# Optimization experiments

Hardware: AMD Instinct MI355X
Metric: run time of the kernel (lower is better)

The kernel has to match this reference:

```python
import jax, jax.numpy as jnp
import numpy as np

HEADS, DIM_HEAD = 4, 32
EAF_LAMBDA, EAF_ZMAX = 1.0, 4.0
MIN_SIGMA, MAX_SIGMA = 1.0, 8.0

def _gen_grid(h, w):
    xs = np.linspace(0.0, 1.0, w, dtype=np.float32)
    ys = np.linspace(0.0, 1.0, h, dtype=np.float32)
    gy, gx = np.meshgrid(ys, xs, indexing='ij')
    return np.stack([gx, gy, np.ones_like(gx)], 0)  # [3,h,w]

def setup_inputs():
    key = jax.random.key(0)
    ks = jax.random.split(key, 12)
    B, N, C, D = 4, 6, 128, 128
    Hb, Wb, fh, fw = 25, 25, 24, 48
    inner = HEADS * DIM_HEAD
    # BEV ego-plane grid (same math as BEVEmbedding with bev 200x200, 100m, 3 decoder blocks)
    g = _gen_grid(Hb, Wb)
    g[0] *= 200.0
    g[1] *= 200.0
    V = np.array([[0., -2., 100.], [-2., 0., 100.], [0., 0., 1.]], dtype=np.float32)
    bev_grid = (np.linalg.inv(V) @ g.reshape(3, -1)).reshape(3, Hb, Wb)
    # image plane pixel grid (buffer), scaled to 480x224 image
    ip = _gen_grid(fh, fw)[None]
    ip[:, 0] *= 480.0
    ip[:, 1] *= 224.0
    # cam->world extrinsics: 6 surround cameras on a ring
    E_inv = np.zeros((B, N, 4, 4), dtype=np.float32)
    for n in range(N):
        yaw = 2.0 * np.pi * n / N
        c, s = np.cos(yaw), np.sin(yaw)
        E_inv[:, n, :3, :3] = np.array([[c, -s, 0.], [s, c, 0.], [0., 0., 1.]], dtype=np.float32)
        E_inv[:, n, :3, 3] = np.array([2. * c, 2. * s, 1.6], dtype=np.float32)
        E_inv[:, n, 3, 3] = 1.0
    Kmat = np.array([[260., 0., 240.], [0., 260., 112.], [0., 0., 1.]], dtype=np.float32)
    I_inv = np.broadcast_to(np.linalg.inv(Kmat), (B, N, 3, 3)).astype(np.float32).copy()
    w = lambda k, shape: 0.02 * jax.random.normal(k, shape, dtype=jnp.float32)
    return dict(
        x=jax.random.normal(ks[0], (B, D, Hb, Wb), dtype=jnp.float32),
        feature=jax.random.normal(ks[1], (B, N, C, fh, fw), dtype=jnp.float32),
        I_inv=jnp.asarray(I_inv), E_inv=jnp.asarray(E_inv),
        bev_grid=jnp.asarray(bev_grid), image_plane=jnp.asarray(ip),
        bn_v_g=jnp.ones(C), bn_v_b=jnp.zeros(C), bn_v_m=jnp.zeros(C), bn_v_var=jnp.ones(C),
        conv_v_w=w(ks[2], (D, C)),
        bn_k_g=jnp.ones(C), bn_k_b=jnp.zeros(C), bn_k_m=jnp.zeros(C), bn_k_var=jnp.ones(C),
        conv_k_w=w(ks[3], (D, C)),
        ln_q_g=jnp.ones(D), ln_q_b=jnp.zeros(D),
        ln_k_g=jnp.ones(D), ln_k_b=jnp.zeros(D),
        ln_v_g=jnp.ones(D), ln_v_b=jnp.zeros(D),
        Wq=w(ks[4], (inner, D)), bq=jnp.zeros(inner),
        Wk=w(ks[5], (inner, D)), bk=jnp.zeros(inner),
        Wv=w(ks[6], (inner, D)), bv=jnp.zeros(inner),
        Wo=w(ks[7], (D, inner)), bo=jnp.zeros(D),
        ln_pre_g=jnp.ones(D), ln_pre_b=jnp.zeros(D),
        W1=w(ks[8], (2 * D, D)), b1=jnp.zeros(2 * D),
        W2=w(ks[9], (D, 2 * D)), b2=jnp.zeros(D),
        ln_post_g=jnp.ones(D), ln_post_b=jnp.zeros(D),
    )

def _ln(x, g, b):
    m = x.mean(-1, keepdims=True)
    v = ((x - m) ** 2).mean(-1, keepdims=True)
    return (x - m) * jax.lax.rsqrt(v + 1e-5) * g + b

def _bn_relu_conv(f, g, b, mu, var, Wc):
    # inference BatchNorm2d -> ReLU -> 1x1 Conv (no bias)
    f = (f - mu[None, :, None, None]) * (jax.lax.rsqrt(var + 1e-5) * g)[None, :, None, None] + b[None, :, None, None]
    f = jax.nn.relu(f)
    return jnp.einsum('bchw,dc->bdhw', f, Wc)

def reference(x, feature, I_inv, E_inv, bev_grid, image_plane,
              bn_v_g, bn_v_b, bn_v_m, bn_v_var, conv_v_w,
              bn_k_g, bn_k_b, bn_k_m, bn_k_var, conv_k_w,
              ln_q_g, ln_q_b, ln_k_g, ln_k_b, ln_v_g, ln_v_b,
              Wq, bq, Wk, bk, Wv, bv, Wo, bo,
              ln_pre_g, ln_pre_b, W1, b1, W2, b2, ln_post_g, ln_post_b):
    B, N, C, fh, fw = feature.shape
    _, D, Hb, Wb = x.shape
    Q = Hb * Wb
    Kp = fh * fw
    feat = feature.reshape(B * N, C, fh, fw)
    val = _bn_relu_conv(feat, bn_v_g, bn_v_b, bn_v_m, bn_v_var, conv_v_w)
    keyf = _bn_relu_conv(feat, bn_k_g, bn_k_b, bn_k_m, bn_k_var, conv_k_w)
    v = val.reshape(B, N, D, fh, fw)
    k = keyf.reshape(B, N, D, fh, fw)
    # ---- EAF weights ----
    xy = bev_grid[:2].reshape(2, Q).T                      # [Q,2]
    ones = jnp.ones((Q, 1), dtype=bev_grid.dtype)
    P0 = jnp.concatenate([xy, 0.0 * ones, ones], -1)       # [Q,4] z=0
    P1 = jnp.concatenate([xy, EAF_ZMAX * ones, ones], -1)  # [Q,4] z=zmax
    E = jnp.linalg.inv(E_inv)                              # world->cam
    P0c = jnp.einsum('bnij,qj->bnqi', E, P0)
    P1c = jnp.einsum('bnij,qj->bnqi', E, P1)
    Icam = jnp.linalg.inv(I_inv)
    p0 = jnp.einsum('bnij,bnqj->bnqi', Icam, P0c[..., :3])
    p1 = jnp.einsum('bnij,bnqj->bnqi', Icam, P1c[..., :3])
    p0 = p0 / (p0[..., 2:3] + 1e-8)
    p1 = p1 / (p1[..., 2:3] + 1e-8)
    l = jnp.cross(p0, p1)                                  # epipolar line [B,N,Q,3]
    denom = jnp.maximum(jnp.sqrt(l[..., 0] ** 2 + l[..., 1] ** 2), 1e-8)
    l_hat = l / denom[..., None]
    x_img = image_plane[0].reshape(3, Kp).T                # [K,3]
    d = jnp.abs(jnp.einsum('bnqj,kj->bnqk', l_hat, x_img))
    # adaptive lambda_{q,i}
    cam_xy = E_inv[..., :2, 3]                             # [B,N,2]
    vec = xy[None, None] - cam_xy[:, :, None]              # [B,N,Q,2]
    dist = jnp.linalg.norm(vec, axis=-1) + 1e-6
    dist_max = dist.max(axis=(1, 2), keepdims=True) + 1e-6
    dist_norm = jnp.clip(dist / dist_max, 0.0, 1.0)
    sigma = MAX_SIGMA - dist_norm * (MAX_SIGMA - MIN_SIGMA)
    lambda_qi = 1.0 / (sigma + 1e-6)
    scale_w = (EAF_LAMBDA * lambda_qi) ** 2                # [B,N,Q]
    Wmask = jnp.exp(-scale_w[..., None] * d ** 2)          # [B,N,Q,K]
    W_logits = Wmask.transpose(0, 2, 1, 3).reshape(B, Q, N * Kp)
    # ---- cross attention (EAF weight multiplied into logits pre-softmax) ----
    qt = x.reshape(B, D, Q).transpose(0, 2, 1)             # [B,Q,D]
    kt = k.transpose(0, 1, 3, 4, 2).reshape(B, N * Kp, D)
    vt = v.transpose(0, 1, 3, 4, 2).reshape(B, N * Kp, D)
    qp = _ln(qt, ln_q_g, ln_q_b) @ Wq.T + bq
    kp = _ln(kt, ln_k_g, ln_k_b) @ Wk.T + bk
    vp = _ln(vt, ln_v_g, ln_v_b) @ Wv.T + bv
    qh = qp.reshape(B, Q, HEADS, DIM_HEAD).transpose(0, 2, 1, 3)
    kh = kp.reshape(B, N * Kp, HEADS, DIM_HEAD).transpose(0, 2, 1, 3)
    vh = vp.reshape(B, N * Kp, HEADS, DIM_HEAD).transpose(0, 2, 1, 3)
    logits = jnp.einsum('bhqd,bhkd->bhqk', qh, kh) * (DIM_HEAD ** -0.5)
    logits = logits * W_logits[:, None]                    # broadcast over heads
    attn = jax.nn.softmax(logits, axis=-1)
    out = jnp.einsum('bhqk,bhkd->bhqd', attn, vh)
    out = out.transpose(0, 2, 1, 3).reshape(B, Q, HEADS * DIM_HEAD)
    out = out @ Wo.T + bo                                  # [B,Q,D]
    z = out + qt                                           # skip = x
    z = _ln(z, ln_pre_g, ln_pre_b)
    z = z + (jax.nn.gelu(z @ W1.T + b1, approximate=False) @ W2.T + b2)
    z = _ln(z, ln_post_g, ln_post_b)
    return z.transpose(0, 2, 1).reshape(B, D, Hb, Wb)
```

## Files before the change

kernel.cpp:

```cpp
#include <hip/hip_runtime.h>
#include <hip/hip_bf16.h>

typedef unsigned short u16;
typedef __attribute__((ext_vector_type(8))) short short8v;
typedef __attribute__((ext_vector_type(4))) float f32x4;
typedef __attribute__((ext_vector_type(2))) __fp16 fp16x2;

#define B_   4
#define N_   6
#define Q_   625
#define QPAD 640
#define KP_  1152
#define NK_  6912
#define NKB  216
#define NSPLIT 12
#define KSEG (NK_/NSPLIT)
#define FHW  1152
#define LOG2E 1.4426950408889634f
#define LOG2_LOG2E 0.5287663729448977f

__device__ __forceinline__ float bfu(unsigned int u16v){ return __uint_as_float(u16v << 16); }
__device__ __forceinline__ unsigned int f2bfu(float f){
  unsigned int u = __float_as_uint(f);
  return (u + 0x7fffu + ((u>>16)&1u)) >> 16;
// ... 110 lines not shown
    for (int j=0;j<4;++j) a[i][4+j] = (i==j)?1.f:0.f;
  }
  #pragma unroll
  for (int col=0;col<4;++col){
    float inv = 1.f/a[col][col];
    #pragma unroll
    for (int j=0;j<8;++j) a[col][j]*=inv;
    #pragma unroll
    for (int rr=0;rr<4;++rr) if (rr!=col){
      float f=a[rr][col];
      #pragma unroll
      for (int j=0;j<8;++j) a[rr][j] -= f*a[col][j];
    }
  }
  float E[3][4];
  #pragma unroll
  for (int i=0;i<3;++i)
    #pragma unroll
    for (int j=0;j<4;++j) E[i][j]=a[i][4+j];

  float m9[9];
  #pragma unroll
  for (int i=0;i<9;++i) m9[i] = Iinv[(b*N_+n)*9 + i];
  float c00 =  m9[4]*m9[8]-m9[5]*m9[7];
  float c01 = -(m9[3]*m9[8]-m9[5]*m9[6]);
  float c02 =  m9[3]*m9[7]-m9[4]*m9[6];
  float id = 1.f/(m9[0]*c00 + m9[1]*c01 + m9[2]*c02);
  float Ic[3][3];
  Ic[0][0]=c00*id; Ic[0][1]=-(m9[1]*m9[8]-m9[2]*m9[7])*id; Ic[0][2]=(m9[1]*m9[5]-m9[2]*m9[4])*id;
  Ic[1][0]=c01*id; Ic[1][1]= (m9[0]*m9[8]-m9[2]*m9[6])*id; Ic[1][2]=-(m9[0]*m9[5]-m9[2]*m9[3])*id;
  Ic[2][0]=c02*id; Ic[2][1]=-(m9[0]*m9[7]-m9[1]*m9[6])*id; Ic[2][2]=(m9[0]*m9[4]-m9[1]*m9[3])*id;

  float x = bev[q], y = bev[Q_+q];
  float P0c[3], P1c[3];
  #pragma unroll
  for (int i=0;i<3;++i){
    P0c[i] = E[i][0]*x + E[i][1]*y + E[i][3];
    P1c[i] = E[i][0]*x + E[i][1]*y + E[i][2]*4.0f + E[i][3];
  }
  float p0[3], p1[3];
  #pragma unroll
  for (int i=0;i<3;++i){
    p0[i] = Ic[i][0]*P0c[0] + Ic[i][1]*P0c[1] + Ic[i][2]*P0c[2];
    p1[i] = Ic[i][0]*P1c[0] + Ic[i][1]*P1c[1] + Ic[i][2]*P1c[2];
  }
  float z0 = p0[2]+1e-8f, z1 = p1[2]+1e-8f;
  #pragma unroll
  for (int i=0;i<3;++i){ p0[i]/=z0; p1[i]/=z1; }
  float l0 = p0[1]*p1[2]-p0[2]*p1[1];
  float l1 = p0[2]*p1[0]-p0[0]*p1[2];
  float l2 = p0[0]*p1[1]-p0[1]*p1[0];
  float den = fmaxf(sqrtf(l0*l0+l1*l1), 1e-8f);
  float cx = Einv[(b*N_+n)*16+3], cy = Einv[(b*N_+n)*16+7];
  float dx = x-cx, dy = y-cy;
  float dist = sqrtf(dx*dx+dy*dy) + 1e-6f;
  float dn = fminf(fmaxf(dist/dmax[b], 0.f), 1.f);
  float sigma = 8.0f - dn*7.0f;
  float lam = 1.f/(sigma+1e-6f);
  float* g = geom + (size_t)idx*4;
  g[0]=l0/den; g[1]=l1/den; g[2]=l2/den;
  g[3]=-(lam*lam)*LOG2E;
}

__global__ __launch_bounds__(256) void k_kvproj(
  const void* __restrict__ feat, const unsigned* __restrict__ magic,
  const float* __restrict__ csK, const float* __restrict__ cbK,
  const float* __restrict__ csV, const float* __restrict__ cbV,
  const u16* __restrict__ convKbf, const u16* __restrict__ convVbf,
  const u16* __restrict__ WkBf, const u16* __restrict__ WvBf,
  const float* __restrict__ lkg, const float* __restrict__ lkb,
  const float* __restrict__ lvg, const float* __restrict__ lvb,
  const float* __restrict__ bk_, const float* __restrict__ bv_,
  u16* __restrict__ kp, u16* __restrict__ vpB)
{
  __shared__ __align__(16) unsigned char lds_tile[16384];
  __shared__ float2 redLN[4][64];
  uint4* lds16 = reinterpret_cast<uint4*>(lds_tile);

  const int tid = threadIdx.x;
  const int w = tid >> 6, l = tid & 63;
  const int lr = l & 15, lg4 = l >> 4;
  const int ptile = blockIdx.x;
  const int bn = blockIdx.y, b = bn/6, n = bn - b*6;
  const int half = blockIdx.z;
  const bool isbf = (*magic == 0x3F803F80u);

  const float* cs   = half ? csV : csK;
  const float* cbv_ = half ? cbV : cbK;
  const u16* convB  = half ? convVbf : convKbf;
  const u16* WB     = half ? WvBf : WkBf;
  const float* lng  = half ? lvg : lkg;
  const float* lnb  = half ? lvb : lkb;
  const float* bias = half ? bv_ : bk_;

  const size_t fbase = (size_t)bn*128*FHW + ptile*64 + l;
  const int psw = l & 7;
  #pragma unroll
  for (int pass=0; pass<4; ++pass){
    int c0 = pass*32 + w*8;
    unsigned int u[4];
    #pragma unroll
    for (int i2=0;i2<4;++i2){
      int ca = c0 + i2*2, cb2 = ca+1;
      float fa = ldfeat(feat, fbase + (size_t)ca*FHW, isbf);
      float fb = ldfeat(feat, fbase + (size_t)cb2*FHW, isbf);
      float aa = fmaxf(fa*cs[ca]+cbv_[ca], 0.f);
      float ab = fmaxf(fb*cs[cb2]+cbv_[cb2], 0.f);
      u[i2] = f2bfu(aa) | (f2bfu(ab)<<16);
    }
    int c8 = c0 >> 3;
    lds16[l*16 + (c8 ^ psw)] = make_uint4(u[0],u[1],u[2],u[3]);
  }
  __syncthreads();

  f32x4 acc[2][4];
  #pragma unroll
  for (int i=0;i<2;++i)
    #pragma unroll
    for (int j=0;j<4;++j) acc[i][j] = (f32x4){0.f,0.f,0.f,0.f};

  #pragma unroll
  for (int ks2=0; ks2<4; ++ks2){
    short8v af[2];
    #pragma unroll
    for (int ib=0; ib<2; ++ib)
      af[ib] = *reinterpret_cast<const short8v*>(convB + ((w*32 + ib*16 + lr)<<7) + (ks2<<5) + (lg4<<3));
    #pragma unroll
    for (int pb2=0; pb2<4; ++pb2){
      int p = pb2*16 + lr;
      U4S8 bu; bu.u = lds16[p*16 + ((ks2*4 + lg4) ^ (p&7))];
      acc[0][pb2] = __builtin_amdgcn_mfma_f32_16x16x32_bf16(af[0], bu.s, acc[0][pb2], 0,0,0);
      acc[1][pb2] = __builtin_amdgcn_mfma_f32_16x16x32_bf16(af[1], bu.s, acc[1][pb2], 0,0,0);
    }
  }

  float s1v[4], s2v[4];
  #pragma unroll
  for (int pb2=0;pb2<4;++pb2){
    float s=0.f, s2=0.f;
    #pragma unroll
    for (int ib=0;ib<2;++ib)
      #pragma unroll
      for (int r=0;r<4;++r){ float v = acc[ib][pb2][r]; s+=v; s2+=v*v; }
    s += __shfl_xor(s,16);  s += __shfl_xor(s,32);
    s2 += __shfl_xor(s2,16); s2 += __shfl_xor(s2,32);
    s1v[pb2]=s; s2v[pb2]=s2;
  }
  if (l < 16){
    #pragma unroll
    for (int pb2=0;pb2<4;++pb2) redLN[w][pb2*16+l] = make_float2(s1v[pb2], s2v[pb2]);
  }
  __syncthreads();

  float mean[4], rstd[4];
  #pragma unroll
  for (int pb2=0;pb2<4;++pb2){
    int p = pb2*16 + lr;
    float2 t0 = redLN[0][p], t1 = redLN[1][p], t2 = redLN[2][p], t3 = redLN[3][p];
    float S = t0.x+t1.x+t2.x+t3.x, S2 = t0.y+t1.y+t2.y+t3.y;
    float mm = S*(1.f/128.f);
    float var = fmaxf(S2*(1.f/128.f) - mm*mm, 0.f);
    mean[pb2] = mm; rstd[pb2] = rsqrtf(var + 1e-5f);
  }
  float4 g4[2], b4[2];
  #pragma unroll
  for (int ib=0;ib<2;++ib){
    g4[ib] = *reinterpret_cast<const float4*>(lng + w*32 + ib*16 + lg4*4);
    b4[ib] = *reinterpret_cast<const float4*>(lnb + w*32 + ib*16 + lg4*4);
  }
  #pragma unroll
  for (int ib=0;ib<2;++ib){
    const float* gg = &g4[ib].x; const float* bb2 = &b4[ib].x;
    int d0 = w*32 + ib*16 + lg4*4;
    int d8 = d0 >> 3, doff = (d0 & 7) * 2;
    #pragma unroll
    for (int pb2=0;pb2<4;++pb2){
      int p = pb2*16 + lr;
      float z0 = (acc[ib][pb2][0]-mean[pb2])*rstd[pb2]*gg[0]+bb2[0];
      float z1 = (acc[ib][pb2][1]-mean[pb2])*rstd[pb2]*gg[1]+bb2[1];
      float z2 = (acc[ib][pb2][2]-mean[pb2])*rstd[pb2]*gg[2]+bb2[2];
      float z3 = (acc[ib][pb2][3]-mean[pb2])*rstd[pb2]*gg[3]+bb2[3];
      unsigned int u0 = f2bfu(z0) | (f2bfu(z1)<<16);
      unsigned int u1 = f2bfu(z2) | (f2bfu(z3)<<16);
      *reinterpret_cast<uint2*>(lds_tile + p*256 + ((d8 ^ (p&7))<<4) + doff) = make_uint2(u0,u1);
    }
  }
  __syncthreads();

  f32x4 acc2[2][4];
  #pragma unroll
  for (int i=0;i<2;++i)
    #pragma unroll
    for (int j=0;j<4;++j) acc2[i][j] = (f32x4){0.f,0.f,0.f,0.f};

  #pragma unroll
  for (int ks2=0; ks2<4; ++ks2){
    short8v af[2];
    #pragma unroll
    for (int ib=0; ib<2; ++ib)
      af[ib] = *reinterpret_cast<const short8v*>(WB + ((w*32 + ib*16 + lr)<<7) + (ks2<<5) + (lg4<<3));
    #pragma unroll
    for (int pb2=0; pb2<4; ++pb2){
      int p = pb2*16 + lr;
      U4S8 bu; bu.u = lds16[p*16 + ((ks2*4 + lg4) ^ (p&7))];
      acc2[0][pb2] = __builtin_amdgcn_mfma_f32_16x16x32_bf16(af[0], bu.s, acc2[0][pb2], 0,0,0);
      acc2[1][pb2] = __builtin_amdgcn_mfma_f32_16x16x32_bf16(af[1], bu.s, acc2[1][pb2], 0,0,0);
    }
  }
  float4 bias4[2];
  #pragma unroll
  for (int ib=0;ib<2;++ib)
    bias4[ib] = *reinterpret_cast<const float4*>(bias + w*32 + ib*16 + lg4*4);

  __syncthreads();

  if (half == 0){
    #pragma unroll
    for (int ib=0;ib<2;++ib){
      const float* bb2 = &bias4[ib].x;
      int i0 = w*32 + ib*16 + lg4*4;
      int i8 = i0 >> 3, ioff = (i0 & 7) * 2;
      #pragma unroll
      for (int pb2=0;pb2<4;++pb2){
        int p = pb2*16 + lr;
        unsigned int u0 = f2bfu(acc2[ib][pb2][0]+bb2[0]) | (f2bfu(acc2[ib][pb2][1]+bb2[1])<<16);
        unsigned int u1 = f2bfu(acc2[ib][pb2][2]+bb2[2]) | (f2bfu(acc2[ib][pb2][3]+bb2[3])<<16);
        *reinterpret_cast<uint2*>(lds_tile + p*256 + ((i8 ^ (p&7))<<4) + ioff) = make_uint2(u0,u1);
      }
    }
    __syncthreads();
    size_t krow0 = (size_t)b*NK_ + n*KP_ + ptile*64;
    #pragma unroll
    for (int kk=0;kk<4;++kk){
      int idx = kk*256 + tid;
      int p = idx >> 4, j = idx & 15;
      uint4 vv = lds16[p*16 + (j ^ (p&7))];
      *reinterpret_cast<uint4*>(kp + (krow0 + p)*128 + j*8) = vv;
    }
  } else {
    u16* lds2 = reinterpret_cast<u16*>(lds_tile);
    #pragma unroll
    for (int ib=0;ib<2;++ib){
      const float* bb2 = &bias4[ib].x;
      int i0 = w*32 + ib*16 + lg4*4;
      #pragma unroll
      for (int pb2=0;pb2<4;++pb2){
        int p = pb2*16 + lr;
        int pc = ((p&12)<<1) | (p&3) | ((p&16)>>2) | (p&32);
        #pragma unroll
        for (int r=0;r<4;++r)
          lds2[(i0+r)*64 + pc] = (u16)f2bfu(acc2[ib][pb2][r]+bb2[r]);
      }
    }
    __syncthreads();
    int kb0 = b*NKB + n*(KP_/32) + ptile*2;
    #pragma unroll
    for (int kk=0;kk<4;++kk){
      int idx = kk*256 + tid;
      int p2 = idx >> 9, d = (idx>>2)&127, ch = idx&3;
      uint4 vv = lds16[d*8 + p2*4 + ch];
      *reinterpret_cast<uint4*>(vpB + ((size_t)(kb0+p2)*128 + d)*32 + ch*8) = vv;
    }
  }
}

__global__ __launch_bounds__(256) void k_qprojM(
  const float* __restrict__ x, const float* __restrict__ lg, const float* __restrict__ lb,
  const u16* __restrict__ WqBf, const float* __restrict__ bq_, u16* __restrict__ qp)
{
  const float SCL = 0.17677669529663687f;
  __shared__ __align__(16) unsigned char lds_tile[16384];
  __shared__ float redS[4][64], redS2[4][64];
  uint4* lds16 = reinterpret_cast<uint4*>(lds_tile);

  const int tid = threadIdx.x;
  const int w = tid >> 6, l = tid & 63;
  const int lr = l & 15, lg4 = l >> 4;
  const int q0 = blockIdx.x * 64;
  const int b  = blockIdx.y;

  int qg = q0 + l; if (qg > Q_-1) qg = Q_-1;
  float xv[32];
  float s = 0.f, s2 = 0.f;
  #pragma unroll
  for (int i=0;i<32;++i){
    float v = x[(size_t)(b*128 + w*32 + i)*Q_ + qg];
    xv[i] = v; s += v; s2 += v*v;
  }
  redS[w][l] = s; redS2[w][l] = s2;
  __syncthreads();
  float S  = redS[0][l]+redS[1][l]+redS[2][l]+redS[3][l];
  float S2 = redS2[0][l]+redS2[1][l]+redS2[2][l]+redS2[3][l];
  float mm = S*(1.f/128.f);
  float rs = rsqrtf(fmaxf(S2*(1.f/128.f)-mm*mm, 0.f) + 1e-5f);
  #pragma unroll
  for (int j=0;j<4;++j){
    unsigned u[4];
    #pragma unroll
    for (int c2=0;c2<4;++c2){
      int i = j*8 + c2*2;
      int d = w*32 + i;
      float z0 = (xv[i]  -mm)*rs*lg[d]   + lb[d];
      float z1 = (xv[i+1]-mm)*rs*lg[d+1] + lb[d+1];
      u[c2] = f2bfu(z0) | (f2bfu(z1)<<16);
    }
    int d8 = w*4 + j;
    lds16[l*16 + (d8 ^ (l&7))] = make_uint4(u[0],u[1],u[2],u[3]);
  }
  __syncthreads();

  f32x4 acc2[2][4];
  #pragma unroll
  for (int i=0;i<2;++i)
    #pragma unroll
    for (int j=0;j<4;++j) acc2[i][j] = (f32x4){0.f,0.f,0.f,0.f};

  #pragma unroll
  for (int ks2=0; ks2<4; ++ks2){
    short8v af[2];
    #pragma unroll
    for (int ib=0; ib<2; ++ib)
      af[ib] = *reinterpret_cast<const short8v*>(WqBf + ((w*32 + ib*16 + lr)<<7) + (ks2<<5) + (lg4<<3));
    #pragma unroll
    for (int pb2=0; pb2<4; ++pb2){
      int p = pb2*16 + lr;
      U4S8 bu; bu.u = lds16[p*16 + ((ks2*4 + lg4) ^ (p&7))];
      acc2[0][pb2] = __builtin_amdgcn_mfma_f32_16x16x32_bf16(af[0], bu.s, acc2[0][pb2], 0,0,0);
      acc2[1][pb2] = __builtin_amdgcn_mfma_f32_16x16x32_bf16(af[1], bu.s, acc2[1][pb2], 0,0,0);
    }
  }
  float4 bias4[2];
  #pragma unroll
  for (int ib=0;ib<2;++ib)
    bias4[ib] = *reinterpret_cast<const float4*>(bq_ + w*32 + ib*16 + lg4*4);

  __syncthreads();
  #pragma unroll
  for (int ib=0;ib<2;++ib){
    const float* bb2 = &bias4[ib].x;
    int i0 = w*32 + ib*16 + lg4*4;
    int i8 = i0 >> 3, ioff = (i0 & 7) * 2;
    #pragma unroll
    for (int pb2=0;pb2<4;++pb2){
      int p = pb2*16 + lr;
      unsigned int u0 = f2bfu((acc2[ib][pb2][0]+bb2[0])*SCL) | (f2bfu((acc2[ib][pb2][1]+bb2[1])*SCL)<<16);
      unsigned int u1 = f2bfu((acc2[ib][pb2][2]+bb2[2])*SCL) | (f2bfu((acc2[ib][pb2][3]+bb2[3])*SCL)<<16);
      *reinterpret_cast<uint2*>(lds_tile + p*256 + ((i8 ^ (p&7))<<4) + ioff) = make_uint2(u0,u1);
    }
  }
  __syncthreads();
  #pragma unroll
  for (int kk=0;kk<4;++kk){
    int idx = kk*256 + tid;
    int p = idx >> 4, j = idx & 15;
    uint4 vv = lds16[p*16 + (j ^ (p&7))];
    *reinterpret_cast<uint4*>(qp + (size_t)(b*QPAD + q0 + p)*128 + j*8) = vv;
  }
}

__global__ __launch_bounds__(256) void k_attn(
    const u16* __restrict__ qp, const u16* __restrict__ kp, const u16* __restrict__ vpB,
    const float* __restrict__ geom, const float* __restrict__ ip,
    float* __restrict__ part)
{
  __shared__ uint4 ldsK[2][512];
  __shared__ uint4 ldsV[2][512];
  __shared__ u16  ldsW[2][32*36];

  const int tid = threadIdx.x;
  const int h = tid >> 6;
  const int lane = tid & 63;
  const int lq = lane & 15;
  const int g  = lane >> 4;
  const int bid = blockIdx.x;
  const int b = bid / (20*NSPLIT);
  const int r = bid - b*(20*NSPLIT);
  const int qt = r / NSPLIT;
  const int ks = r - qt*NSPLIT;
  const int q0 = qt*32;
  const int qa = q0 + lq;
  const int qb = q0 + 16 + lq;

  short8v bq0 = *reinterpret_cast<const short8v*>(qp + ((size_t)(b*QPAD + qa))*128 + h*32 + g*8);
  short8v bq1 = *reinterpret_cast<const short8v*>(qp + ((size_t)(b*QPAD + qb))*128 + h*32 + g*8);

  f32x4 o00={0,0,0,0}, o01={0,0,0,0}, o10={0,0,0,0}, o11={0,0,0,0};
  f32x4 zero4 = {0.f,0.f,0.f,0.f};
  float psum0 = 0.f, psum1 = 0.f;

  const int kbeg = ks*KSEG, kend = kbeg + KSEG;
  const int n0 = kbeg / KP_;
  const int pb0 = kbeg - n0*KP_;

  const int wq = tid >> 3, wc = tid & 7;
  int qwg = q0 + wq; if (qwg > Q_-1) qwg = Q_-1;
  const float* gw_ = geom + ((size_t)((b*N_+n0)*Q_ + qwg))*4;
  const float wl0 = gw_[0], wl1 = gw_[1], wl2 = gw_[2], wgw = gw_[3];

  const int c2 = tid*2;
  const int kr0 = c2 >> 4, kch = c2 & 15;
  const int vd0 = c2 >> 2, vch = c2 & 3;
  const int vsw = (vd0 >> 1) & 3;
  auto STAGE = [&](int buf, int k0){
    const uint4* gk = reinterpret_cast<const uint4*>(kp + (size_t)(b*NK_ + k0)*128);
    uint4 k0v = gk[c2], k1v = gk[c2+1];
    ldsK[buf][kr0*16 + (kch     ^ (kr0&7))] = k0v;
    ldsK[buf][kr0*16 + ((kch+1) ^ (kr0&7))] = k1v;
    const uint4* gv = reinterpret_cast<const uint4*>(vpB + ((size_t)(b*NKB + (k0>>5))*128)*32);
    uint4 v0v = gv[c2], v1v = gv[c2+1];
    ldsV[buf][vd0*4 + (vch     ^ vsw)] = v0v;
    ldsV[buf][vd0*4 + ((vch+1) ^ vsw)] = v1v;
  };
  auto WSTAGE = [&](int buf, int k0){
    int key = pb0 + (k0 - kbeg) + wc*4;
    float4 xx = *reinterpret_cast<const float4*>(ip + key);
    float4 yy = *reinterpret_cast<const float4*>(ip + KP_ + key);
    const float* xp = &xx.x; const float* yp = &yy.x;
    float wv[4];
    #pragma unroll
    for (int i=0;i<4;++i){
      float dln = fmaf(wl0, xp[i], fmaf(wl1, yp[i], wl2));
      wv[i] = exp2a(fmaf(wgw, dln*dln, LOG2_LOG2E));
    }
    uint2 pk;
    pk.x = cvtpk_f16(wv[0], wv[1]);
    pk.y = cvtpk_f16(wv[2], wv[3]);
    *reinterpret_cast<uint2*>(&ldsW[buf][wq*36 + wc*4]) = pk;
  };

  STAGE(0, kbeg);
  WSTAGE(0, kbeg);

  int cur = 0;
  const int kchunk = h*4 + g;
  const int dd = h*32 + lq;
  const int vswr = (dd >> 1) & 3;
  for (int k0 = kbeg; k0 < kend; k0 += 32){
    __syncthreads();
    bool more = (k0 + 32) < kend;
    if (more){ STAGE(cur^1, k0+32); WSTAGE(cur^1, k0+32); }

    uint2 wA0 = *reinterpret_cast<const uint2*>(&ldsW[cur][lq*36 + g*4]);
    uint2 wA1 = *reinterpret_cast<const uint2*>(&ldsW[cur][lq*36 + 16 + g*4]);
    uint2 wB0 = *reinterpret_cast<const uint2*>(&ldsW[cur][(16+lq)*36 + g*4]);
    uint2 wB1 = *reinterpret_cast<const uint2*>(&ldsW[cur][(16+lq)*36 + 16 + g*4]);
    float w00[4], w01[4], w10[4], w11[4];
    {
      H2U t0,t1,t2,t3,t4,t5,t6,t7;
      t0.u=wA0.x; t1.u=wA0.y; t2.u=wA1.x; t3.u=wA1.y;
      t4.u=wB0.x; t5.u=wB0.y; t6.u=wB1.x; t7.u=wB1.y;
      w00[0]=(float)t0.h[0]; w00[1]=(float)t0.h[1]; w00[2]=(float)t1.h[0]; w00[3]=(float)t1.h[1];
      w01[0]=(float)t2.h[0]; w01[1]=(float)t2.h[1]; w01[2]=(float)t3.h[0]; w01[3]=(float)t3.h[1];
      w10[0]=(float)t4.h[0]; w10[1]=(float)t4.h[1]; w10[2]=(float)t5.h[0]; w10[3]=(float)t5.h[1];
      w11[0]=(float)t6.h[0]; w11[1]=(float)t6.h[1]; w11[2]=(float)t7.h[0]; w11[3]=(float)t7.h[1];
    }

    __builtin_amdgcn_s_setprio(1);
    U4S8 a0, a1;
    a0.u = ldsK[cur][lq*16      + (kchunk ^ (lq&7))];
    a1.u = ldsK[cur][(16+lq)*16 + (kchunk ^ (lq&7))];
    f32x4 s00 = __builtin_amdgcn_mfma_f32_16x16x32_bf16(a0.s, bq0, zero4, 0,0,0);
    f32x4 s01 = __builtin_amdgcn_mfma_f32_16x16x32_bf16(a1.s, bq0, zero4, 0,0,0);
    f32x4 s10 = __builtin_amdgcn_mfma_f32_16x16x32_bf16(a0.s, bq1, zero4, 0,0,0);
    f32x4 s11 = __builtin_amdgcn_mfma_f32_16x16x32_bf16(a1.s, bq1, zero4, 0,0,0);

    float p00[4], p01[4], p10[4], p11[4];
    #pragma unroll
    for (int r2=0;r2<4;++r2){
      p00[r2] = exp2a(fmaf(s00[r2], w00[r2], -8.f));
      p01[r2] = exp2a(fmaf(s01[r2], w01[r2], -8.f));
      psum0 += p00[r2] + p01[r2];
      p10[r2] = exp2a(fmaf(s10[r2], w10[r2], -8.f));
      p11[r2] = exp2a(fmaf(s11[r2], w11[r2], -8.f));
      psum1 += p10[r2] + p11[r2];
    }
    union { short8v s; unsigned int u[4]; } bp0, bp1;
    bp0.u[0] = cvtpk_bf16(p00[0], p00[1]);
    bp0.u[1] = cvtpk_bf16(p00[2], p00[3]);
    bp0.u[2] = cvtpk_bf16(p01[0], p01[1]);
    bp0.u[3] = cvtpk_bf16(p01[2], p01[3]);
    bp1.u[0] = cvtpk_bf16(p10[0], p10[1]);
    bp1.u[1] = cvtpk_bf16(p10[2], p10[3]);
    bp1.u[2] = cvtpk_bf16(p11[0], p11[1]);
    bp1.u[3] = cvtpk_bf16(p11[2], p11[3]);

    U4S8 v0, v1;
    v0.u = ldsV[cur][dd*4      + (g ^ vswr)];
    v1.u = ldsV[cur][(dd+16)*4 + (g ^ vswr)];
    o00 = __builtin_amdgcn_mfma_f32_16x16x32_bf16(v0.s, bp0.s, o00, 0,0,0);
    o01 = __builtin_amdgcn_mfma_f32_16x16x32_bf16(v1.s, bp0.s, o01, 0,0,0);
    o10 = __builtin_amdgcn_mfma_f32_16x16x32_bf16(v0.s, bp1.s, o10, 0,0,0);
    o11 = __builtin_amdgcn_mfma_f32_16x16x32_bf16(v1.s, bp1.s, o11, 0,0,0);
    __builtin_amdgcn_s_setprio(0);

    cur ^= 1;
  }
  psum0 += __shfl_xor(psum0,16);
  psum0 += __shfl_xor(psum0,32);
  psum1 += __shfl_xor(psum1,16);
  psum1 += __shfl_xor(psum1,32);
  int slot0 = ((b*4 + h)*40 + qt*2    )*NSPLIT + ks;
  int slot1 = ((b*4 + h)*40 + qt*2 + 1)*NSPLIT + ks;
  float* pr0 = part + ((size_t)slot0*16 + lq)*34;
  float* pr1 = part + ((size_t)slot1*16 + lq)*34;
  #pragma unroll
  for (int r2=0;r2<4;++r2){
    pr0[g*4+r2] = o00[r2]; pr0[16+g*4+r2] = o01[r2];
    pr1[g*4+r2] = o10[r2]; pr1[16+g*4+r2] = o11[r2];
  }
  if (g==0){ pr0[33] = psum0; pr1[33] = psum1; }
}

__global__ __launch_bounds__(256) void k_epiM(
  const float* __restrict__ part, const float* __restrict__ x,
  const u16* __restrict__ WoBf, const float* __restrict__ bo_,
  const float* __restrict__ lpg, const float* __restrict__ lpb,
  const u16* __restrict__ W1Bf, const float* __restrict__ b1_,
  const u16* __restrict__ W2Bf, const float* __restrict__ b2_,
  const float* __restrict__ lsg, const float* __restrict__ lsb,
  void* __restrict__ out, const unsigned* __restrict__ magic)
{
  const float ISQ2 = 0.7071067811865476f;
  __shared__ __align__(16) unsigned char lds_tile[16384];
  __shared__ __align__(16) unsigned char lds_h1[32768];
  __shared__ float2 redLN[4][64];
  uint4* lds16 = reinterpret_cast<uint4*>(lds_tile);
  uint4* ldsH  = reinterpret_cast<uint4*>(lds_h1);

  const int tid = threadIdx.x;
  const int w = tid >> 6, l = tid & 63;
  const int lr = l & 15, lg4 = l >> 4;
  const int q0 = blockIdx.x * 64;
  const int b  = blockIdx.y;
  const bool isbf = (*magic == 0x3F803F80u);

  {
    int qg = q0 + l; if (qg > Q_-1) qg = Q_-1;
    int qt = qg >> 4, qq = qg & 15;
    const float* base = part + (size_t)(((b*4+w)*40+qt)*NSPLIT)*544 + qq*34;
    float den = 0.f;
    #pragma unroll
    for (int s=0;s<NSPLIT;++s) den += base[s*544 + 33];
    float rden = 1.f/den;
    float num[32];
    #pragma unroll
    for (int i=0;i<32;++i) num[i]=0.f;
    #pragma unroll
    for (int s=0;s<NSPLIT;++s){
      const float* bp = base + s*544;
      #pragma unroll
      for (int i=0;i<32;++i) num[i] += bp[i];
    }
    #pragma unroll
    for (int j=0;j<4;++j){
      unsigned u[4];
      #pragma unroll
      for (int c2=0;c2<4;++c2){
        int i = j*8 + c2*2;
        u[c2] = f2bfu(num[i]*rden) | (f2bfu(num[i+1]*rden)<<16);
      }
      int d8 = w*4 + j;
      lds16[l*16 + (d8 ^ (l&7))] = make_uint4(u[0],u[1],u[2],u[3]);
    }
  }
  __syncthreads();

  f32x4 acc[2][4];
  #pragma unroll
  for (int i=0;i<2;++i)
    #pragma unroll
    for (int j=0;j<4;++j) acc[i][j] = (f32x4){0.f,0.f,0.f,0.f};
  #pragma unroll
  for (int ks2=0; ks2<4; ++ks2){
    short8v af[2];
    #pragma unroll
    for (int ib=0; ib<2; ++ib)
      af[ib] = *reinterpret_cast<const short8v*>(WoBf + ((w*32 + ib*16 + lr)<<7) + (ks2<<5) + (lg4<<3));
// ... 202 lines not shown
  InPack P;
  int nseg = n_in < 38 ? n_in : 38;
  int c = 0;
  for (int i=0;i<nseg;++i){
    P.p[i] = d_in[i];
    P.off[i] = c;
    P.sz[i] = (i == 1) ? 0 : in_sizes[i];
    c += (P.sz[i] + 7) & ~7;
  }
  P.nseg = nseg;
  P.total = c;

  float* fw = (float*)d_ws;
  float* fin = fw;
  const float* fx    = fin + P.off[0];
  const float* fIinv = fin + P.off[2];
  const float* fEinv = fin + P.off[3];
  const float* fbev  = fin + P.off[4];
  const float* fip   = fin + P.off[5];
  const float* fbvg  = fin + P.off[6];
  const float* fbvb  = fin + P.off[7];
  const float* fbvm  = fin + P.off[8];
  const float* fbvv  = fin + P.off[9];
  const float* fcvw  = fin + P.off[10];
  const float* fbkg  = fin + P.off[11];
  const float* fbkb  = fin + P.off[12];
  const float* fbkm  = fin + P.off[13];
  const float* fbkv  = fin + P.off[14];
  const float* fckw  = fin + P.off[15];
  const float* flqg  = fin + P.off[16];
  const float* flqb  = fin + P.off[17];
  const float* flkg  = fin + P.off[18];
  const float* flkb  = fin + P.off[19];
  const float* flvg  = fin + P.off[20];
  const float* flvb  = fin + P.off[21];
  const float* fWq   = fin + P.off[22];
  const float* fbq   = fin + P.off[23];
  const float* fWk   = fin + P.off[24];
  const float* fbk   = fin + P.off[25];
  const float* fWv   = fin + P.off[26];
  const float* fbv   = fin + P.off[27];
  const float* fWo   = fin + P.off[28];
  const float* fbo   = fin + P.off[29];
  const float* flpg  = fin + P.off[30];
  const float* flpb  = fin + P.off[31];
  const float* fW1   = fin + P.off[32];
  const float* fb1   = fin + P.off[33];
  const float* fW2   = fin + P.off[34];
  const float* fb2   = fin + P.off[35];
  const float* flsg  = fin + P.off[36];
  const float* flsb  = fin + P.off[37];

  size_t off = (size_t)P.total;
  float* geomW = fin + off;  off += 60000;
  float* dmaxW = fin + off;  off += 8;
  float* csK = fin + off;    off += 128;
  float* cbK = fin + off;    off += 128;
  float* csV = fin + off;    off += 128;
  float* cbV = fin + off;    off += 128;
  float* part = fin + off;   off += (size_t)B_*4*40*NSPLIT*544;
  u16* bb = (u16*)(fin + off);
  u16* convKbf = bb;
  u16* convVbf = bb + 16384;
  u16* WkBf    = bb + 32768;
  u16* WvBf    = bb + 49152;
  u16* WqBf    = bb + 65536;
  u16* WoBf    = bb + 81920;
  u16* W1Bf    = bb + 98304;
  u16* W2Bf    = bb + 131072;
  u16* kp  = bb + 163840;
  u16* vpB = kp + (size_t)B_*NK_*128;
  u16* qp  = vpB + (size_t)B_*NK_*128;

  const unsigned* magic = (const unsigned*)d_in[6];
  const void* featRaw = d_in[1];

  k_ingest<<<(P.total+255)/256,256,0,stream>>>(P, fin, magic);
  k_prep<<<641,256,0,stream>>>(fckw,fcvw,fWk,fWv,fWq,fWo,fW1,fW2,
                               fbkg,fbkb,fbkm,fbkv, fbvg,fbvb,fbvm,fbvv,
                               convKbf,convVbf,WkBf,WvBf,WqBf,WoBf,W1Bf,W2Bf,
                               csK,cbK,csV,cbV);
  k_distmax<<<4,256,0,stream>>>(fbev, fEinv, dmaxW);
  k_geom<<<59,256,0,stream>>>(fEinv, fIinv, fbev, dmaxW, geomW);
  k_kvproj<<<dim3(18,24,2),256,0,stream>>>(featRaw, magic, csK,cbK,csV,cbV, convKbf,convVbf,
                                           WkBf,WvBf, flkg,flkb,flvg,flvb, fbk,fbv, kp, vpB);
  k_qprojM<<<dim3(10,B_),256,0,stream>>>(fx, flqg,flqb, WqBf, fbq, qp);
  k_attn<<<B_*20*NSPLIT,256,0,stream>>>(qp, kp, vpB, geomW, fip, part);
  k_epiM<<<dim3(10,B_),256,0,stream>>>(part, fx, WoBf,fbo, flpg,flpb, W1Bf,fb1, W2Bf,fb2,
                                       flsg,flsb, d_out, magic);
}
```

Measured before the change: 105.0 us.

## Merge K/V projection blocks to reuse feature loads; read V from global in attention

The K/V projection kernel now runs one block per tile that loops over both halves. It loads the 128-channel feature column into registers once instead of twice, which halves feature reads but halves the grid size and serialises the two projections. In the attention kernel, the LDS staging buffer for V is removed. Each lane now loads its V fragment directly from the pre-swizzled global layout, prefetched one iteration ahead in registers. This cuts LDS traffic and shared memory but leans on cache hits for V.

```diff
diff --git a/kernel.cpp b/kernel.cpp
--- a/kernel.cpp
+++ b/kernel.cpp
@@ -216,185 +216,194 @@
   const int lr = l & 15, lg4 = l >> 4;
   const int ptile = blockIdx.x;
   const int bn = blockIdx.y, b = bn/6, n = bn - b*6;
-  const int half = blockIdx.z;
   const bool isbf = (*magic == 0x3F803F80u);
 
-  const float* cs   = half ? csV : csK;
-  const float* cbv_ = half ? cbV : cbK;
-  const u16* convB  = half ? convVbf : convKbf;
-  const u16* WB     = half ? WvBf : WkBf;
-  const float* lng  = half ? lvg : lkg;
-  const float* lnb  = half ? lvb : lkb;
-  const float* bias = half ? bv_ : bk_;
-
   const size_t fbase = (size_t)bn*128*FHW + ptile*64 + l;
+  float fv[32];
+  #pragma unroll
+  for (int pass=0; pass<4; ++pass)
+    #pragma unroll
+    for (int j=0;j<8;++j){
+      int c = pass*32 + w*8 + j;
+      fv[pass*8+j] = ldfeat(feat, fbase + (size_t)c*FHW, isbf);
+    }
+
   const int psw = l & 7;
-  #pragma unroll
-  for (int pass=0; pass<4; ++pass){
-    int c0 = pass*32 + w*8;
-    unsigned int u[4];
-    #pragma unroll
-    for (int i2=0;i2<4;++i2){
-      int ca = c0 + i2*2, cb2 = ca+1;
-      float fa = ldfeat(feat, fbase + (size_t)ca*FHW, isbf);
-      float fb = ldfeat(feat, fbase + (size_t)cb2*FHW, isbf);
-      float aa = fmaxf(fa*cs[ca]+cbv_[ca], 0.f);
-      float ab = fmaxf(fb*cs[cb2]+cbv_[cb2], 0.f);
-      u[i2] = f2bfu(aa) | (f2bfu(ab)<<16);
-    }
-    int c8 = c0 >> 3;
-    lds16[l*16 + (c8 ^ psw)] = make_uint4(u[0],u[1],u[2],u[3]);
-  }
-  __syncthreads();
-
-  f32x4 acc[2][4];
-  #pragma unroll
-  for (int i=0;i<2;++i)
-    #pragma unroll
-    for (int j=0;j<4;++j) acc[i][j] = (f32x4){0.f,0.f,0.f,0.f};
-
-  #pragma unroll
-  for (int ks2=0; ks2<4; ++ks2){
-    short8v af[2];
-    #pragma unroll
-    for (int ib=0; ib<2; ++ib)
-      af[ib] = *reinterpret_cast<const short8v*>(convB + ((w*32 + ib*16 + lr)<<7) + (ks2<<5) + (lg4<<3));
-    #pragma unroll
-    for (int pb2=0; pb2<4; ++pb2){
-      int p = pb2*16 + lr;
-      U4S8 bu; bu.u = lds16[p*16 + ((ks2*4 + lg4) ^ (p&7))];
-      acc[0][pb2] = __builtin_amdgcn_mfma_f32_16x16x32_bf16(af[0], bu.s, acc[0][pb2], 0,0,0);
-      acc[1][pb2] = __builtin_amdgcn_mfma_f32_16x16x32_bf16(af[1], bu.s, acc[1][pb2], 0,0,0);
-    }
-  }
-
-  float s1v[4], s2v[4];
-  #pragma unroll
-  for (int pb2=0;pb2<4;++pb2){
-    float s=0.f, s2=0.f;
-    #pragma unroll
-    for (int ib=0;ib<2;++ib)
-      #pragma unroll
-      for (int r=0;r<4;++r){ float v = acc[ib][pb2][r]; s+=v; s2+=v*v; }
-    s += __shfl_xor(s,16);  s += __shfl_xor(s,32);
-    s2 += __shfl_xor(s2,16); s2 += __shfl_xor(s2,32);
-    s1v[pb2]=s; s2v[pb2]=s2;
-  }
-  if (l < 16){
-    #pragma unroll
-    for (int pb2=0;pb2<4;++pb2) redLN[w][pb2*16+l] = make_float2(s1v[pb2], s2v[pb2]);
-  }
-  __syncthreads();
-
-  float mean[4], rstd[4];
-  #pragma unroll
-  for (int pb2=0;pb2<4;++pb2){
-    int p = pb2*16 + lr;
-    float2 t0 = redLN[0][p], t1 = redLN[1][p], t2 = redLN[2][p], t3 = redLN[3][p];
-    float S = t0.x+t1.x+t2.x+t3.x, S2 = t0.y+t1.y+t2.y+t3.y;
-    float mm = S*(1.f/128.f);
-    float var = fmaxf(S2*(1.f/128.f) - mm*mm, 0.f);
-    mean[pb2] = mm; rstd[pb2] = rsqrtf(var + 1e-5f);
-  }
-  float4 g4[2], b4[2];
-  #pragma unroll
-  for (int ib=0;ib<2;++ib){
-    g4[ib] = *reinterpret_cast<const float4*>(lng + w*32 + ib*16 + lg4*4);
-    b4[ib] = *reinterpret_cast<const float4*>(lnb + w*32 + ib*16 + lg4*4);
-  }
-  #pragma unroll
-  for (int ib=0;ib<2;++ib){
-    const float* gg = &g4[ib].x; const float* bb2 = &b4[ib].x;
-    int d0 = w*32 + ib*16 + lg4*4;
-    int d8 = d0 >> 3, doff = (d0 & 7) * 2;
+  for (int half=0; half<2; ++half){
+    const float* cs   = half ? csV : csK;
+    const float* cbv_ = half ? cbV : cbK;
+    const u16* convB  = half ? convVbf : convKbf;
+    const u16* WB     = half ? WvBf : WkBf;
+    const float* lng  = half ? lvg : lkg;
+    const float* lnb  = half ? lvb : lkb;
+    const float* bias = half ? bv_ : bk_;
+
+    #pragma unroll
+    for (int pass=0; pass<4; ++pass){
+      int c0 = pass*32 + w*8;
+      unsigned int u[4];
+      #pragma unroll
+      for (int i2=0;i2<4;++i2){
+        int ca = c0 + i2*2, cb2 = ca+1;
+        float aa = fmaxf(fv[pass*8+i2*2  ]*cs[ca]+cbv_[ca], 0.f);
+        float ab = fmaxf(fv[pass*8+i2*2+1]*cs[cb2]+cbv_[cb2], 0.f);
+        u[i2] = f2bfu(aa) | (f2bfu(ab)<<16);
+      }
+      int c8 = c0 >> 3;
+      lds16[l*16 + (c8 ^ psw)] = make_uint4(u[0],u[1],u[2],u[3]);
+    }
+    __syncthreads();
+
+    f32x4 acc[2][4];
+    #pragma unroll
+    for (int i=0;i<2;++i)
+      #pragma unroll
+      for (int j=0;j<4;++j) acc[i][j] = (f32x4){0.f,0.f,0.f,0.f};
+
+    #pragma unroll
+    for (int ks2=0; ks2<4; ++ks2){
+      short8v af[2];
+      #pragma unroll
+      for (int ib=0; ib<2; ++ib)
+        af[ib] = *reinterpret_cast<const short8v*>(convB + ((w*32 + ib*16 + lr)<<7) + (ks2<<5) + (lg4<<3));
+      #pragma unroll
+      for (int pb2=0; pb2<4; ++pb2){
+        int p = pb2*16 + lr;
+        U4S8 bu; bu.u = lds16[p*16 + ((ks2*4 + lg4) ^ (p&7))];
+        acc[0][pb2] = __builtin_amdgcn_mfma_f32_16x16x32_bf16(af[0], bu.s, acc[0][pb2], 0,0,0);
+        acc[1][pb2] = __builtin_amdgcn_mfma_f32_16x16x32_bf16(af[1], bu.s, acc[1][pb2], 0,0,0);
+      }
+    }
+
+    float s1v[4], s2v[4];
+    #pragma unroll
+    for (int pb2=0;pb2<4;++pb2){
+      float s=0.f, s2=0.f;
+      #pragma unroll
+      for (int ib=0;ib<2;++ib)
+        #pragma unroll
+        for (int r=0;r<4;++r){ float v = acc[ib][pb2][r]; s+=v; s2+=v*v; }
+      s += __shfl_xor(s,16);  s += __shfl_xor(s,32);
+      s2 += __shfl_xor(s2,16); s2 += __shfl_xor(s2,32);
+      s1v[pb2]=s; s2v[pb2]=s2;
+    }
+    if (l < 16){
+      #pragma unroll
+      for (int pb2=0;pb2<4;++pb2) redLN[w][pb2*16+l] = make_float2(s1v[pb2], s2v[pb2]);
+    }
+    __syncthreads();
+
+    float mean[4], rstd[4];
     #pragma unroll
     for (int pb2=0;pb2<4;++pb2){
       int p = pb2*16 + lr;
-      float z0 = (acc[ib][pb2][0]-mean[pb2])*rstd[pb2]*gg[0]+bb2[0];
-      float z1 = (acc[ib][pb2][1]-mean[pb2])*rstd[pb2]*gg[1]+bb2[1];
-      float z2 = (acc[ib][pb2][2]-mean[pb2])*rstd[pb2]*gg[2]+bb2[2];
-      float z3 = (acc[ib][pb2][3]-mean[pb2])*rstd[pb2]*gg[3]+bb2[3];
-      unsigned int u0 = f2bfu(z0) | (f2bfu(z1)<<16);
-      unsigned int u1 = f2bfu(z2) | (f2bfu(z3)<<16);
-      *reinterpret_cast<uint2*>(lds_tile + p*256 + ((d8 ^ (p&7))<<4) + doff) = make_uint2(u0,u1);
-    }
-  }
-  __syncthreads();
-
-  f32x4 acc2[2][4];
-  #pragma unroll
-  for (int i=0;i<2;++i)
-    #pragma unroll
-    for (int j=0;j<4;++j) acc2[i][j] = (f32x4){0.f,0.f,0.f,0.f};
-
-  #pragma unroll
-  for (int ks2=0; ks2<4; ++ks2){
-    short8v af[2];
-    #pragma unroll
-    for (int ib=0; ib<2; ++ib)
-      af[ib] = *reinterpret_cast<const short8v*>(WB + ((w*32 + ib*16 + lr)<<7) + (ks2<<5) + (lg4<<3));
-    #pragma unroll
-    for (int pb2=0; pb2<4; ++pb2){
-      int p = pb2*16 + lr;
-      U4S8 bu; bu.u = lds16[p*16 + ((ks2*4 + lg4) ^ (p&7))];
-      acc2[0][pb2] = __builtin_amdgcn_mfma_f32_16x16x32_bf16(af[0], bu.s, acc2[0][pb2], 0,0,0);
-      acc2[1][pb2] = __builtin_amdgcn_mfma_f32_16x16x32_bf16(af[1], bu.s, acc2[1][pb2], 0,0,0);
-    }
-  }
-  float4 bias4[2];
-  #pragma unroll
-  for (int ib=0;ib<2;++ib)
-    bias4[ib] = *reinterpret_cast<const float4*>(bias + w*32 + ib*16 + lg4*4);
-
-  __syncthreads();
-
-  if (half == 0){
+      float2 t0 = redLN[0][p], t1 = redLN[1][p], t2 = redLN[2][p], t3 = redLN[3][p];
+      float S = t0.x+t1.x+t2.x+t3.x, S2 = t0.y+t1.y+t2.y+t3.y;
+      float mm = S*(1.f/128.f);
+      float var = fmaxf(S2*(1.f/128.f) - mm*mm, 0.f);
+      mean[pb2] = mm; rstd[pb2] = rsqrtf(var + 1e-5f);
+    }
+    float4 g4[2], b4[2];
     #pragma unroll
     for (int ib=0;ib<2;++ib){
-      const float* bb2 = &bias4[ib].x;
-      int i0 = w*32 + ib*16 + lg4*4;
-      int i8 = i0 >> 3, ioff = (i0 & 7) * 2;
+      g4[ib] = *reinterpret_cast<const float4*>(lng + w*32 + ib*16 + lg4*4);
+      b4[ib] = *reinterpret_cast<const float4*>(lnb + w*32 + ib*16 + lg4*4);
+    }
+    #pragma unroll
+    for (int ib=0;ib<2;++ib){
+      const float* gg = &g4[ib].x; const float* bb2 = &b4[ib].x;
+      int d0 = w*32 + ib*16 + lg4*4;
+      int d8 = d0 >> 3, doff = (d0 & 7) * 2;
       #pragma unroll
       for (int pb2=0;pb2<4;++pb2){
         int p = pb2*16 + lr;
-        unsigned int u0 = f2bfu(acc2[ib][pb2][0]+bb2[0]) | (f2bfu(acc2[ib][pb2][1]+bb2[1])<<16);
-        unsigned int u1 = f2bfu(acc2[ib][pb2][2]+bb2[2]) | (f2bfu(acc2[ib][pb2][3]+bb2[3])<<16);
-        *reinterpret_cast<uint2*>(lds_tile + p*256 + ((i8 ^ (p&7))<<4) + ioff) = make_uint2(u0,u1);
+        float z0 = (acc[ib][pb2][0]-mean[pb2])*rstd[pb2]*gg[0]+bb2[0];
+        float z1 = (acc[ib][pb2][1]-mean[pb2])*rstd[pb2]*gg[1]+bb2[1];
+        float z2 = (acc[ib][pb2][2]-mean[pb2])*rstd[pb2]*gg[2]+bb2[2];
+        float z3 = (acc[ib][pb2][3]-mean[pb2])*rstd[pb2]*gg[3]+bb2[3];
+        unsigned int u0 = f2bfu(z0) | (f2bfu(z1)<<16);
+        unsigned int u1 = f2bfu(z2) | (f2bfu(z3)<<16);
+        *reinterpret_cast<uint2*>(lds_tile + p*256 + ((d8 ^ (p&7))<<4) + doff) = make_uint2(u0,u1);
       }
     }
     __syncthreads();
-    size_t krow0 = (size_t)b*NK_ + n*KP_ + ptile*64;
-    #pragma unroll
-    for (int kk=0;kk<4;++kk){
-      int idx = kk*256 + tid;
-      int p = idx >> 4, j = idx & 15;
-      uint4 vv = lds16[p*16 + (j ^ (p&7))];
-      *reinterpret_cast<uint4*>(kp + (krow0 + p)*128 + j*8) = vv;
-    }
-  } else {
-    u16* lds2 = reinterpret_cast<u16*>(lds_tile);
-    #pragma unroll
-    for (int ib=0;ib<2;++ib){
-      const float* bb2 = &bias4[ib].x;
-      int i0 = w*32 + ib*16 + lg4*4;
-      #pragma unroll
-      for (int pb2=0;pb2<4;++pb2){
+
+    f32x4 acc2[2][4];
+    #pragma unroll
+    for (int i=0;i<2;++i)
+      #pragma unroll
+      for (int j=0;j<4;++j) acc2[i][j] = (f32x4){0.f,0.f,0.f,0.f};
+
+    #pragma unroll
+    for (int ks2=0; ks2<4; ++ks2){
+      short8v af[2];
+      #pragma unroll
+      for (int ib=0; ib<2; ++ib)
+        af[ib] = *reinterpret_cast<const short8v*>(WB + ((w*32 + ib*16 + lr)<<7) + (ks2<<5) + (lg4<<3));
+      #pragma unroll
+      for (int pb2=0; pb2<4; ++pb2){
         int p = pb2*16 + lr;
-        int pc = ((p&12)<<1) | (p&3) | ((p&16)>>2) | (p&32);
+        U4S8 bu; bu.u = lds16[p*16 + ((ks2*4 + lg4) ^ (p&7))];
+        acc2[0][pb2] = __builtin_amdgcn_mfma_f32_16x16x32_bf16(af[0], bu.s, acc2[0][pb2], 0,0,0);
+        acc2[1][pb2] = __builtin_amdgcn_mfma_f32_16x16x32_bf16(af[1], bu.s, acc2[1][pb2], 0,0,0);
+      }
+    }
+    float4 bias4[2];
+    #pragma unroll
+    for (int ib=0;ib<2;++ib)
+      bias4[ib] = *reinterpret_cast<const float4*>(bias + w*32 + ib*16 + lg4*4);
+
+    __syncthreads();
+
+    if (half == 0){
+      #pragma unroll
+      for (int ib=0;ib<2;++ib){
+        const float* bb2 = &bias4[ib].x;
+        int i0 = w*32 + ib*16 + lg4*4;
+        int i8 = i0 >> 3, ioff = (i0 & 7) * 2;
         #pragma unroll
-        for (int r=0;r<4;++r)
-          lds2[(i0+r)*64 + pc] = (u16)f2bfu(acc2[ib][pb2][r]+bb2[r]);
+        for (int pb2=0;pb2<4;++pb2){
+          int p = pb2*16 + lr;
+          unsigned int u0 = f2bfu(acc2[ib][pb2][0]+bb2[0]) | (f2bfu(acc2[ib][pb2][1]+bb2[1])<<16);
+          unsigned int u1 = f2bfu(acc2[ib][pb2][2]+bb2[2]) | (f2bfu(acc2[ib][pb2][3]+bb2[3])<<16);
+          *reinterpret_cast<uint2*>(lds_tile + p*256 + ((i8 ^ (p&7))<<4) + ioff) = make_uint2(u0,u1);
+        }
+      }
+      __syncthreads();
+      size_t krow0 = (size_t)b*NK_ + n*KP_ + ptile*64;
+      #pragma unroll
+      for (int kk=0;kk<4;++kk){
+        int idx = kk*256 + tid;
+        int p = idx >> 4, j = idx & 15;
+        uint4 vv = lds16[p*16 + (j ^ (p&7))];
+        *reinterpret_cast<uint4*>(kp + (krow0 + p)*128 + j*8) = vv;
+      }
+    } else {
+      u16* lds2 = reinterpret_cast<u16*>(lds_tile);
+      #pragma unroll
+      for (int ib=0;ib<2;++ib){
+        const float* bb2 = &bias4[ib].x;
+        int i0 = w*32 + ib*16 + lg4*4;
+        #pragma unroll
+        for (int pb2=0;pb2<4;++pb2){
+          int p = pb2*16 + lr;
+          int pc = ((p&12)<<1) | (p&3) | ((p&16)>>2) | (p&32);
+          #pragma unroll
+          for (int r=0;r<4;++r)
+            lds2[(i0+r)*64 + pc] = (u16)f2bfu(acc2[ib][pb2][r]+bb2[r]);
+        }
+      }
+      __syncthreads();
+      int kb0 = b*NKB + n*(KP_/32) + ptile*2;
+      #pragma unroll
+      for (int kk=0;kk<4;++kk){
+        int idx = kk*256 + tid;
+        int p2 = idx >> 9, d = (idx>>2)&127, ch = idx&3;
+        uint4 vv = lds16[d*8 + p2*4 + ch];
+        *reinterpret_cast<uint4*>(vpB + ((size_t)(kb0+p2)*128 + d)*32 + ch*8) = vv;
       }
     }
     __syncthreads();
-    int kb0 = b*NKB + n*(KP_/32) + ptile*2;
-    #pragma unroll
-    for (int kk=0;kk<4;++kk){
-      int idx = kk*256 + tid;
-      int p2 = idx >> 9, d = (idx>>2)&127, ch = idx&3;
-      uint4 vv = lds16[d*8 + p2*4 + ch];
-      *reinterpret_cast<uint4*>(vpB + ((size_t)(kb0+p2)*128 + d)*32 + ch*8) = vv;
-    }
   }
 }
 
@@ -498,7 +507,6 @@
     float* __restrict__ part)
 {
   __shared__ uint4 ldsK[2][512];
-  __shared__ uint4 ldsV[2][512];
   __shared__ u16  ldsW[2][32*36];
 
   const int tid = threadIdx.x;
@@ -533,17 +541,11 @@
 
   const int c2 = tid*2;
   const int kr0 = c2 >> 4, kch = c2 & 15;
-  const int vd0 = c2 >> 2, vch = c2 & 3;
-  const int vsw = (vd0 >> 1) & 3;
   auto STAGE = [&](int buf, int k0){
     const uint4* gk = reinterpret_cast<const uint4*>(kp + (size_t)(b*NK_ + k0)*128);
     uint4 k0v = gk[c2], k1v = gk[c2+1];
     ldsK[buf][kr0*16 + (kch     ^ (kr0&7))] = k0v;
     ldsK[buf][kr0*16 + ((kch+1) ^ (kr0&7))] = k1v;
-    const uint4* gv = reinterpret_cast<const uint4*>(vpB + ((size_t)(b*NKB + (k0>>5))*128)*32);
-    uint4 v0v = gv[c2], v1v = gv[c2+1];
-    ldsV[buf][vd0*4 + (vch     ^ vsw)] = v0v;
-    ldsV[buf][vd0*4 + ((vch+1) ^ vsw)] = v1v;
   };
   auto WSTAGE = [&](int buf, int k0){
     int key = pb0 + (k0 - kbeg) + wc*4;
@@ -562,17 +564,25 @@
     *reinterpret_cast<uint2*>(&ldsW[buf][wq*36 + wc*4]) = pk;
   };
 
+  const uint4* vpb4 = reinterpret_cast<const uint4*>(vpB);
+  const int dd = h*32 + lq;
+  const int iv0 = dd*4 + g, iv1 = (dd+16)*4 + g;
+  auto VPAN = [&](int k0){ return vpb4 + ((size_t)(b*NKB + (k0>>5)))*512; };
+
   STAGE(0, kbeg);
   WSTAGE(0, kbeg);
+  U4S8 vc0, vc1;
+  { const uint4* vp = VPAN(kbeg); vc0.u = vp[iv0]; vc1.u = vp[iv1]; }
 
   int cur = 0;
   const int kchunk = h*4 + g;
-  const int dd = h*32 + lq;
-  const int vswr = (dd >> 1) & 3;
   for (int k0 = kbeg; k0 < kend; k0 += 32){
     __syncthreads();
     bool more = (k0 + 32) < kend;
     if (more){ STAGE(cur^1, k0+32); WSTAGE(cur^1, k0+32); }
+    int kn = more ? (k0 + 32) : k0;
+    U4S8 vn0, vn1;
+    { const uint4* vp = VPAN(kn); vn0.u = vp[iv0]; vn1.u = vp[iv1]; }
 
     uint2 wA0 = *reinterpret_cast<const uint2*>(&ldsW[cur][lq*36 + g*4]);
     uint2 wA1 = *reinterpret_cast<const uint2*>(&ldsW[cur][lq*36 + 16 + g*4]);
@@ -618,15 +628,13 @@
     bp1.u[2] = cvtpk_bf16(p11[0], p11[1]);
     bp1.u[3] = cvtpk_bf16(p11[2], p11[3]);
 
-    U4S8 v0, v1;
-    v0.u = ldsV[cur][dd*4      + (g ^ vswr)];
-    v1.u = ldsV[cur][(dd+16)*4 + (g ^ vswr)];
-    o00 = __builtin_amdgcn_mfma_f32_16x16x32_bf16(v0.s, bp0.s, o00, 0,0,0);
-    o01 = __builtin_amdgcn_mfma_f32_16x16x32_bf16(v1.s, bp0.s, o01, 0,0,0);
-    o10 = __builtin_amdgcn_mfma_f32_16x16x32_bf16(v0.s, bp1.s, o10, 0,0,0);
-    o11 = __builtin_amdgcn_mfma_f32_16x16x32_bf16(v1.s, bp1.s, o11, 0,0,0);
+    o00 = __builtin_amdgcn_mfma_f32_16x16x32_bf16(vc0.s, bp0.s, o00, 0,0,0);
+    o01 = __builtin_amdgcn_mfma_f32_16x16x32_bf16(vc1.s, bp0.s, o01, 0,0,0);
+    o10 = __builtin_amdgcn_mfma_f32_16x16x32_bf16(vc0.s, bp1.s, o10, 0,0,0);
+    o11 = __builtin_amdgcn_mfma_f32_16x16x32_bf16(vc1.s, bp1.s, o11, 0,0,0);
     __builtin_amdgcn_s_setprio(0);
 
+    vc0 = vn0; vc1 = vn1;
     cur ^= 1;
   }
   psum0 += __shfl_xor(psum0,16);
@@ -995,8 +1003,8 @@
                                csK,cbK,csV,cbV);
   k_distmax<<<4,256,0,stream>>>(fbev, fEinv, dmaxW);
   k_geom<<<59,256,0,stream>>>(fEinv, fIinv, fbev, dmaxW, geomW);
-  k_kvproj<<<dim3(18,24,2),256,0,stream>>>(featRaw, magic, csK,cbK,csV,cbV, convKbf,convVbf,
-                                           WkBf,WvBf, flkg,flkb,flvg,flvb, fbk,fbv, kp, vpB);
+  k_kvproj<<<dim3(18,24),256,0,stream>>>(featRaw, magic, csK,cbK,csV,cbV, convKbf,convVbf,
+                                         WkBf,WvBf, flkg,flkb,flvg,flvb, fbk,fbv, kp, vpB);
   k_qprojM<<<dim3(10,B_),256,0,stream>>>(fx, flqg,flqb, WqBf, fbq, qp);
   k_attn<<<B_*20*NSPLIT,256,0,stream>>>(qp, kp, vpB, geomW, fip, part);
   k_epiM<<<dim3(10,B_),256,0,stream>>>(part, fx, WoBf,fbo, flpg,flpb, W1Bf,fb1, W2Bf,fb2,
```

Result: no change. 103.3 us (-1.6%).
